# Kernel tuning notes

Measured on AMD Instinct MI355X. Metric: run time of the kernel, lower is better.

The kernel has to match this reference:

```python
import jax, jax.numpy as jnp
import numpy as np

K = 3  # knnLoss default k


def _knn_loss(source_pc, target_pc, k=K):
    """Faithful translation of knnLoss.forward.

    For each batch: drop exact-zero (0,0,0) points from both clouds
    (emulated via masking for static shapes), find the k nearest *target*
    points for every *source* point (query=source, ref=target), take the
    mean Euclidean distance, then average over batch.
    """

    def per_batch(src, tgt):  # src, tgt: [N, 3]
        src_valid = jnp.any(src != 0.0, axis=-1)  # [Ns] move_zero_point mask
        tgt_valid = jnp.any(tgt != 0.0, axis=-1)  # [Nt]
        s2 = jnp.sum(src * src, axis=-1)          # [Ns]
        t2 = jnp.sum(tgt * tgt, axis=-1)          # [Nt]
        # squared pairwise distances, [Ns, Nt]
        d2 = s2[:, None] + t2[None, :] - 2.0 * (src @ tgt.T)
        d2 = jnp.maximum(d2, 0.0)
        # invalid (zero) target points can never be a neighbor
        d2 = jnp.where(tgt_valid[None, :], d2, jnp.inf)
        neg_top, _ = jax.lax.top_k(-d2, k)        # k smallest squared dists
        dist = jnp.sqrt(-neg_top)                 # [Ns, k] euclidean, like KNN_CUDA
        # mean over valid source points x k neighbors
        num = jnp.sum(jnp.where(src_valid[:, None], dist, 0.0))
        den = jnp.sum(src_valid).astype(dist.dtype) * k
        return num / den

    return jnp.mean(jax.vmap(per_batch)(source_pc, target_pc))


def setup_inputs() -> dict:
    key = jax.random.key(0)
    k1, k2 = jax.random.split(key)
    B, N = 4, 8192
    source_pc = jax.random.normal(k1, (B, N, 3), dtype=jnp.float32)
    target_pc = jax.random.normal(k2, (B, N, 3), dtype=jnp.float32)
    return {"source_pc": source_pc, "target_pc": target_pc}


def reference(source_pc, target_pc):
    return _knn_loss(source_pc, target_pc)
```

## Files before the change

### kernel.cpp

```cpp
#include <hip/hip_runtime.h>
#include <math.h>

#define BATCH 4
#define NPTS 8192
#define TILE 512
#define TSPLIT 16
#define SRC_PER_BLOCK 512
#define SRC_CHUNKS 16
#define NSRC_TOT (BATCH * NPTS)

typedef __attribute__((ext_vector_type(2))) float f2;

__device__ __forceinline__ void insert3(float d, float& a0, float& a1, float& a2) {
    float h = fmaxf(a1, d);
    float m = __builtin_amdgcn_fmed3f(a0, a1, d);
    a2 = fminf(a2, h);
    a1 = m;
    a0 = fminf(a0, d);
}

__device__ __forceinline__ void merge33(float a0, float a1, float a2,
                                        float& b0, float& b1, float& b2) {
    float s0 = fminf(a0, b0);
    float h  = fmaxf(a0, b0);
    float m  = fminf(a1, b1);
    float mm = fminf(a2, b2);
    b1 = fminf(h, m);
    b2 = __builtin_amdgcn_fmed3f(h, m, mm);
    b0 = s0;
}

__global__ __launch_bounds__(256) void knn_partial(const float* __restrict__ src,
                                                   const float* __restrict__ tgt,
                                                   float* __restrict__ part,
                                                   float* __restrict__ hdr) {
    __shared__ float4 ts[TILE / 2 * 2];
    const int tid = threadIdx.x;
    const int sc = blockIdx.x, tc = blockIdx.y, b = blockIdx.z;

    if (sc == 0 && tc == 0 && b == 0 && tid < 16) hdr[tid] = 0.0f;

    {
        const float* tb = tgt + ((size_t)b * NPTS + (size_t)tc * TILE + 2 * tid) * 3;
        float x0 = tb[0], y0 = tb[1], z0 = tb[2];
        float x1 = tb[3], y1 = tb[4], z1 = tb[5];
        float w0 = x0 * x0 + y0 * y0 + z0 * z0;
        float w1 = x1 * x1 + y1 * y1 + z1 * z1;
        if (!(x0 != 0.f || y0 != 0.f || z0 != 0.f)) w0 = 3.0e38f;
        if (!(x1 != 0.f || y1 != 0.f || z1 != 0.f)) w1 = 3.0e38f;
        ts[2 * tid + 0] = make_float4(x0, x1, y0, y1);
        ts[2 * tid + 1] = make_float4(z0, z1, w0, w1);
    }
    __syncthreads();

    f2 nx[2], ny[2], nz[2], s2[2];
    #pragma unroll
    for (int s = 0; s < 2; ++s) {
        int i = sc * SRC_PER_BLOCK + tid + 256 * s;
        const float* sp = src + ((size_t)b * NPTS + i) * 3;
        float ax = sp[0], ay = sp[1], az = sp[2];
        float q = ax * ax + ay * ay + az * az;
        nx[s] = (f2){-2.f * ax, -2.f * ax};
        ny[s] = (f2){-2.f * ay, -2.f * ay};
        nz[s] = (f2){-2.f * az, -2.f * az};
        s2[s] = (f2){q, q};
    }

    float c0[2][2], c1[2][2], c2[2][2];
    #pragma unroll
    for (int s = 0; s < 2; ++s)
        for (int h = 0; h < 2; ++h) { c0[s][h] = c1[s][h] = c2[s][h] = 3e38f; }

    #pragma unroll 4
    for (int e = 0; e < TILE / 2; ++e) {
        float4 p = ts[2 * e + 0];
        float4 q = ts[2 * e + 1];
        f2 xs = (f2){p.x, p.y};
        f2 ys = (f2){p.z, p.w};
        f2 zs = (f2){q.x, q.y};
        f2 ws = (f2){q.z, q.w};
        #pragma unroll
        for (int s = 0; s < 2; ++s) {
            f2 acc = ws + s2[s];
            acc = __builtin_elementwise_fma(zs, nz[s], acc);
            acc = __builtin_elementwise_fma(ys, ny[s], acc);
            acc = __builtin_elementwise_fma(xs, nx[s], acc);
            insert3(acc.x, c0[s][0], c1[s][0], c2[s][0]);
            insert3(acc.y, c0[s][1], c1[s][1], c2[s][1]);
        }
    }

    #pragma unroll
    for (int s = 0; s < 2; ++s) {
        merge33(c0[s][1], c1[s][1], c2[s][1], c0[s][0], c1[s][0], c2[s][0]);
        size_t flat = (size_t)b * NPTS + sc * SRC_PER_BLOCK + tid + 256 * s;
        part[((size_t)tc * 3 + 0) * NSRC_TOT + flat] = c0[s][0];
        part[((size_t)tc * 3 + 1) * NSRC_TOT + flat] = c1[s][0];
        part[((size_t)tc * 3 + 2) * NSRC_TOT + flat] = c2[s][0];
    }
}

__global__ __launch_bounds__(256) void knn_merge(const float* __restrict__ src,
                                                 const float* __restrict__ part,
                                                 float* __restrict__ acc,
                                                 float* __restrict__ cnt,
                                                 unsigned* __restrict__ ticket,
                                                 float* __restrict__ out) {
    const int gid = blockIdx.x * 256 + threadIdx.x;
    const int b = gid >> 13;

    float t0[4], t1[4], t2[4];
    #pragma unroll
    for (int c = 0; c < 4; ++c) { t0[c] = t1[c] = t2[c] = 3e38f; }
    #pragma unroll
    for (int q = 0; q < TSPLIT * 3; ++q)
        insert3(part[(size_t)q * NSRC_TOT + gid], t0[q & 3], t1[q & 3], t2[q & 3]);
    merge33(t0[1], t1[1], t2[1], t0[0], t1[0], t2[0]);
    merge33(t0[3], t1[3], t2[3], t0[2], t1[2], t2[2]);
    merge33(t0[2], t1[2], t2[2], t0[0], t1[0], t2[0]);

    float sx = src[(size_t)gid * 3 + 0];
    float sy = src[(size_t)gid * 3 + 1];
    float sz = src[(size_t)gid * 3 + 2];
    bool valid = (sx != 0.f) || (sy != 0.f) || (sz != 0.f);
    float s = valid ? (sqrtf(fmaxf(t0[0], 0.f)) + sqrtf(fmaxf(t1[0], 0.f)) +
                       sqrtf(fmaxf(t2[0], 0.f)))
                    : 0.f;
    float c = valid ? 1.f : 0.f;

    for (int off = 32; off >= 1; off >>= 1) {
        s += __shfl_down(s, off);
        c += __shfl_down(c, off);
    }
    __shared__ float red_s[4], red_c[4];
    int wave = threadIdx.x >> 6, lane = threadIdx.x & 63;
    if (lane == 0) { red_s[wave] = s; red_c[wave] = c; }
    __syncthreads();
    if (threadIdx.x == 0) {
        atomicAdd(&acc[b], red_s[0] + red_s[1] + red_s[2] + red_s[3]);
        atomicAdd(&cnt[b], red_c[0] + red_c[1] + red_c[2] + red_c[3]);
        __threadfence();
        unsigned t = atomicAdd(ticket, 1u);
        if (t == (unsigned)(gridDim.x - 1)) {
            float loss = 0.f;
            #pragma unroll
            for (int bb = 0; bb < BATCH; ++bb) {
                float as = atomicAdd(&acc[bb], 0.f);
                float ac = atomicAdd(&cnt[bb], 0.f);
                loss += as / (ac * 3.0f);
            }
            out[0] = loss * (1.0f / BATCH);
        }
    }
}

extern "C" void kernel_launch(void* const* d_in, const int* in_sizes, int n_in,
                              void* d_out, int out_size, void* d_ws, size_t ws_size,
                              hipStream_t stream) {
    const float* src = (const float*)d_in[0];
    const float* tgt = (const float*)d_in[1];
    float* out = (float*)d_out;

    float* hdr = (float*)d_ws;
    float* acc = hdr;
    float* cnt = hdr + 4;
    unsigned* ticket = (unsigned*)((char*)d_ws + 32);
    float* part = (float*)((char*)d_ws + 256);

    dim3 g1(SRC_CHUNKS, TSPLIT, BATCH);
    knn_partial<<<g1, 256, 0, stream>>>(src, tgt, part, hdr);

    knn_merge<<<dim3(NSRC_TOT / 256), 256, 0, stream>>>(src, part, acc, cnt, ticket, out);
}
```

Baseline: 116.1 us.

## Split merge across four waves per source group and defer source norm

The merge kernel now gives each block 64 source points and splits their 48 partial candidate lists across four waves, which combine through shared memory before the final reduction. This spreads the loads and insertion work over four times as many blocks. The source squared norm is also dropped from the inner distance loop of the partial kernel and added back at merge time, removing one vector add per pair. The cost is extra shared-memory traffic, a barrier, and four times as many atomic operations on the accumulators and ticket.

Result: slower. 126.0 us (+8.5%).

```diff
diff --git a/kernel.cpp b/kernel.cpp
--- a/kernel.cpp
+++ b/kernel.cpp
@@ -8,6 +8,9 @@
 #define SRC_PER_BLOCK 512
 #define SRC_CHUNKS 16
 #define NSRC_TOT (BATCH * NPTS)
+#define QTOT (TSPLIT * 3)
+#define QGROUPS 4
+#define QPG (QTOT / QGROUPS)
 
 typedef __attribute__((ext_vector_type(2))) float f2;
 
@@ -53,17 +56,15 @@
     }
     __syncthreads();
 
-    f2 nx[2], ny[2], nz[2], s2[2];
+    f2 nx[2], ny[2], nz[2];
     #pragma unroll
     for (int s = 0; s < 2; ++s) {
         int i = sc * SRC_PER_BLOCK + tid + 256 * s;
         const float* sp = src + ((size_t)b * NPTS + i) * 3;
         float ax = sp[0], ay = sp[1], az = sp[2];
-        float q = ax * ax + ay * ay + az * az;
         nx[s] = (f2){-2.f * ax, -2.f * ax};
         ny[s] = (f2){-2.f * ay, -2.f * ay};
         nz[s] = (f2){-2.f * az, -2.f * az};
-        s2[s] = (f2){q, q};
     }
 
     float c0[2][2], c1[2][2], c2[2][2];
@@ -81,8 +82,7 @@
         f2 ws = (f2){q.z, q.w};
         #pragma unroll
         for (int s = 0; s < 2; ++s) {
-            f2 acc = ws + s2[s];
-            acc = __builtin_elementwise_fma(zs, nz[s], acc);
+            f2 acc = __builtin_elementwise_fma(zs, nz[s], ws);
             acc = __builtin_elementwise_fma(ys, ny[s], acc);
             acc = __builtin_elementwise_fma(xs, nx[s], acc);
             insert3(acc.x, c0[s][0], c1[s][0], c2[s][0]);
@@ -106,50 +106,69 @@
                                                  float* __restrict__ cnt,
                                                  unsigned* __restrict__ ticket,
                                                  float* __restrict__ out) {
-    const int gid = blockIdx.x * 256 + threadIdx.x;
+    const int lane = threadIdx.x & 63;
+    const int qg = threadIdx.x >> 6;
+    const int gid = blockIdx.x * 64 + lane;
     const int b = gid >> 13;
 
-    float t0[4], t1[4], t2[4];
+    float v[QPG];
     #pragma unroll
-    for (int c = 0; c < 4; ++c) { t0[c] = t1[c] = t2[c] = 3e38f; }
+    for (int j = 0; j < QPG; ++j)
+        v[j] = part[(size_t)(qg * QPG + j) * NSRC_TOT + gid];
+
+    float t0[2], t1[2], t2[2];
     #pragma unroll
-    for (int q = 0; q < TSPLIT * 3; ++q)
-        insert3(part[(size_t)q * NSRC_TOT + gid], t0[q & 3], t1[q & 3], t2[q & 3]);
+    for (int c = 0; c < 2; ++c) { t0[c] = t1[c] = t2[c] = 3e38f; }
+    #pragma unroll
+    for (int j = 0; j < QPG; ++j)
+        insert3(v[j], t0[j & 1], t1[j & 1], t2[j & 1]);
     merge33(t0[1], t1[1], t2[1], t0[0], t1[0], t2[0]);
-    merge33(t0[3], t1[3], t2[3], t0[2], t1[2], t2[2]);
-    merge33(t0[2], t1[2], t2[2], t0[0], t1[0], t2[0]);
 
-    float sx = src[(size_t)gid * 3 + 0];
-    float sy = src[(size_t)gid * 3 + 1];
-    float sz = src[(size_t)gid * 3 + 2];
-    bool valid = (sx != 0.f) || (sy != 0.f) || (sz != 0.f);
-    float s = valid ? (sqrtf(fmaxf(t0[0], 0.f)) + sqrtf(fmaxf(t1[0], 0.f)) +
-                       sqrtf(fmaxf(t2[0], 0.f)))
-                    : 0.f;
-    float c = valid ? 1.f : 0.f;
+    __shared__ float r0[QGROUPS][64], r1[QGROUPS][64], r2[QGROUPS][64];
+    r0[qg][lane] = t0[0];
+    r1[qg][lane] = t1[0];
+    r2[qg][lane] = t2[0];
 
-    for (int off = 32; off >= 1; off >>= 1) {
-        s += __shfl_down(s, off);
-        c += __shfl_down(c, off);
+    float sx = 0.f, sy = 0.f, sz = 0.f;
+    if (threadIdx.x < 64) {
+        sx = src[(size_t)gid * 3 + 0];
+        sy = src[(size_t)gid * 3 + 1];
+        sz = src[(size_t)gid * 3 + 2];
     }
-    __shared__ float red_s[4], red_c[4];
-    int wave = threadIdx.x >> 6, lane = threadIdx.x & 63;
-    if (lane == 0) { red_s[wave] = s; red_c[wave] = c; }
     __syncthreads();
-    if (threadIdx.x == 0) {
-        atomicAdd(&acc[b], red_s[0] + red_s[1] + red_s[2] + red_s[3]);
-        atomicAdd(&cnt[b], red_c[0] + red_c[1] + red_c[2] + red_c[3]);
-        __threadfence();
-        unsigned t = atomicAdd(ticket, 1u);
-        if (t == (unsigned)(gridDim.x - 1)) {
-            float loss = 0.f;
-            #pragma unroll
-            for (int bb = 0; bb < BATCH; ++bb) {
-                float as = atomicAdd(&acc[bb], 0.f);
-                float ac = atomicAdd(&cnt[bb], 0.f);
-                loss += as / (ac * 3.0f);
+
+    if (threadIdx.x < 64) {
+        float a0 = r0[0][lane], a1 = r1[0][lane], a2 = r2[0][lane];
+        #pragma unroll
+        for (int g = 1; g < QGROUPS; ++g)
+            merge33(r0[g][lane], r1[g][lane], r2[g][lane], a0, a1, a2);
+
+        bool valid = (sx != 0.f) || (sy != 0.f) || (sz != 0.f);
+        float q2 = sx * sx + sy * sy + sz * sz;
+        float s = valid ? (sqrtf(fmaxf(a0 + q2, 0.f)) + sqrtf(fmaxf(a1 + q2, 0.f)) +
+                           sqrtf(fmaxf(a2 + q2, 0.f)))
+                        : 0.f;
+        float c = valid ? 1.f : 0.f;
+
+        for (int off = 32; off >= 1; off >>= 1) {
+            s += __shfl_down(s, off);
+            c += __shfl_down(c, off);
+        }
+        if (lane == 0) {
+            atomicAdd(&acc[b], s);
+            atomicAdd(&cnt[b], c);
+            __threadfence();
+            unsigned t = atomicAdd(ticket, 1u);
+            if (t == (unsigned)(gridDim.x - 1)) {
+                float loss = 0.f;
+                #pragma unroll
+                for (int bb = 0; bb < BATCH; ++bb) {
+                    float as = atomicAdd(&acc[bb], 0.f);
+                    float ac = atomicAdd(&cnt[bb], 0.f);
+                    loss += as / (ac * 3.0f);
+                }
+                out[0] = loss * (1.0f / BATCH);
             }
-            out[0] = loss * (1.0f / BATCH);
         }
     }
 }
@@ -170,5 +189,5 @@
     dim3 g1(SRC_CHUNKS, TSPLIT, BATCH);
     knn_partial<<<g1, 256, 0, stream>>>(src, tgt, part, hdr);
 
-    knn_merge<<<dim3(NSRC_TOT / 256), 256, 0, stream>>>(src, part, acc, cnt, ticket, out);
+    knn_merge<<<dim3(NSRC_TOT / 64), 256, 0, stream>>>(src, part, acc, cnt, ticket, out);
 }
```

## Prune KNN scan with per-octet minima and rescan top three octets

Applied to the files above, without the earlier changes.

The inner loop now reduces each group of eight target points to a single minimum with v_min3. The octet index is packed into the low mantissa bits, and only these minima go through the top-3 insertion. A second pass then rescans the three winning octets exactly to get the true top-3 per tile. The source squared norm moves out of the hot loop and is added in the merge kernel, which saves one add per pair. The trade-offs are a new shared-memory layout padded to 36 floats per octet and some extra LDS reads in the rescan, plus a small loss of precision in the octet ranking from masking mantissa bits.

Measured after the change: 98.78 us. 1.18x faster.

```diff
diff --git a/kernel.cpp b/kernel.cpp
--- a/kernel.cpp
+++ b/kernel.cpp
@@ -8,8 +8,16 @@
 #define SRC_PER_BLOCK 512
 #define SRC_CHUNKS 16
 #define NSRC_TOT (BATCH * NPTS)
+#define NOCT (TILE / 8)
+#define OCTF 36
 
 typedef __attribute__((ext_vector_type(2))) float f2;
+
+__device__ __forceinline__ float min3f(float a, float b, float c) {
+    float d;
+    asm("v_min3_f32 %0, %1, %2, %3" : "=v"(d) : "v"(a), "v"(b), "v"(c));
+    return d;
+}
 
 __device__ __forceinline__ void insert3(float d, float& a0, float& a1, float& a2) {
     float h = fmaxf(a1, d);
@@ -30,11 +38,37 @@
     b0 = s0;
 }
 
+__device__ __forceinline__ void octet_insert(const float4* ob, f2 nx, f2 ny, f2 nz,
+                                             float& c0, float& c1, float& c2) {
+    float4 X0 = ob[0], X1 = ob[1], Y0 = ob[2], Y1 = ob[3];
+    float4 Z0 = ob[4], Z1 = ob[5], W0 = ob[6], W1 = ob[7];
+    f2 pa = __builtin_elementwise_fma((f2){Z0.x, Z0.y}, nz, (f2){W0.x, W0.y});
+    pa = __builtin_elementwise_fma((f2){Y0.x, Y0.y}, ny, pa);
+    pa = __builtin_elementwise_fma((f2){X0.x, X0.y}, nx, pa);
+    f2 pb = __builtin_elementwise_fma((f2){Z0.z, Z0.w}, nz, (f2){W0.z, W0.w});
+    pb = __builtin_elementwise_fma((f2){Y0.z, Y0.w}, ny, pb);
+    pb = __builtin_elementwise_fma((f2){X0.z, X0.w}, nx, pb);
+    f2 pc = __builtin_elementwise_fma((f2){Z1.x, Z1.y}, nz, (f2){W1.x, W1.y});
+    pc = __builtin_elementwise_fma((f2){Y1.x, Y1.y}, ny, pc);
+    pc = __builtin_elementwise_fma((f2){X1.x, X1.y}, nx, pc);
+    f2 pd = __builtin_elementwise_fma((f2){Z1.z, Z1.w}, nz, (f2){W1.z, W1.w});
+    pd = __builtin_elementwise_fma((f2){Y1.z, Y1.w}, ny, pd);
+    pd = __builtin_elementwise_fma((f2){X1.z, X1.w}, nx, pd);
+    insert3(pa.x, c0, c1, c2);
+    insert3(pa.y, c0, c1, c2);
+    insert3(pb.x, c0, c1, c2);
+    insert3(pb.y, c0, c1, c2);
+    insert3(pc.x, c0, c1, c2);
+    insert3(pc.y, c0, c1, c2);
+    insert3(pd.x, c0, c1, c2);
+    insert3(pd.y, c0, c1, c2);
+}
+
 __global__ __launch_bounds__(256) void knn_partial(const float* __restrict__ src,
                                                    const float* __restrict__ tgt,
                                                    float* __restrict__ part,
                                                    float* __restrict__ hdr) {
-    __shared__ float4 ts[TILE / 2 * 2];
+    __shared__ float tsf[NOCT * OCTF];
     const int tid = threadIdx.x;
     const int sc = blockIdx.x, tc = blockIdx.y, b = blockIdx.z;
 
@@ -48,55 +82,74 @@
         float w1 = x1 * x1 + y1 * y1 + z1 * z1;
         if (!(x0 != 0.f || y0 != 0.f || z0 != 0.f)) w0 = 3.0e38f;
         if (!(x1 != 0.f || y1 != 0.f || z1 != 0.f)) w1 = 3.0e38f;
-        ts[2 * tid + 0] = make_float4(x0, x1, y0, y1);
-        ts[2 * tid + 1] = make_float4(z0, z1, w0, w1);
+        int o = tid >> 2;
+        int k = (2 * tid) & 7;
+        int base = o * OCTF + ((k >> 2) << 2) + (k & 3);
+        *(float2*)(tsf + base)      = make_float2(x0, x1);
+        *(float2*)(tsf + base + 8)  = make_float2(y0, y1);
+        *(float2*)(tsf + base + 16) = make_float2(z0, z1);
+        *(float2*)(tsf + base + 24) = make_float2(w0, w1);
     }
     __syncthreads();
 
-    f2 nx[2], ny[2], nz[2], s2[2];
+    f2 nx[2], ny[2], nz[2];
     #pragma unroll
     for (int s = 0; s < 2; ++s) {
         int i = sc * SRC_PER_BLOCK + tid + 256 * s;
         const float* sp = src + ((size_t)b * NPTS + i) * 3;
         float ax = sp[0], ay = sp[1], az = sp[2];
-        float q = ax * ax + ay * ay + az * az;
         nx[s] = (f2){-2.f * ax, -2.f * ax};
         ny[s] = (f2){-2.f * ay, -2.f * ay};
         nz[s] = (f2){-2.f * az, -2.f * az};
-        s2[s] = (f2){q, q};
-    }
-
-    float c0[2][2], c1[2][2], c2[2][2];
-    #pragma unroll
-    for (int s = 0; s < 2; ++s)
-        for (int h = 0; h < 2; ++h) { c0[s][h] = c1[s][h] = c2[s][h] = 3e38f; }
-
-    #pragma unroll 4
-    for (int e = 0; e < TILE / 2; ++e) {
-        float4 p = ts[2 * e + 0];
-        float4 q = ts[2 * e + 1];
-        f2 xs = (f2){p.x, p.y};
-        f2 ys = (f2){p.z, p.w};
-        f2 zs = (f2){q.x, q.y};
-        f2 ws = (f2){q.z, q.w};
+    }
+
+    float q0[2], q1[2], q2c[2];
+    #pragma unroll
+    for (int s = 0; s < 2; ++s) { q0[s] = q1[s] = q2c[s] = 3e38f; }
+
+    const float4* tsv = (const float4*)tsf;
+    #pragma unroll 2
+    for (int o = 0; o < NOCT; ++o) {
+        float4 X0 = tsv[9 * o + 0], X1 = tsv[9 * o + 1];
+        float4 Y0 = tsv[9 * o + 2], Y1 = tsv[9 * o + 3];
+        float4 Z0 = tsv[9 * o + 4], Z1 = tsv[9 * o + 5];
+        float4 W0 = tsv[9 * o + 6], W1 = tsv[9 * o + 7];
         #pragma unroll
         for (int s = 0; s < 2; ++s) {
-            f2 acc = ws + s2[s];
-            acc = __builtin_elementwise_fma(zs, nz[s], acc);
-            acc = __builtin_elementwise_fma(ys, ny[s], acc);
-            acc = __builtin_elementwise_fma(xs, nx[s], acc);
-            insert3(acc.x, c0[s][0], c1[s][0], c2[s][0]);
-            insert3(acc.y, c0[s][1], c1[s][1], c2[s][1]);
+            f2 pa = __builtin_elementwise_fma((f2){Z0.x, Z0.y}, nz[s], (f2){W0.x, W0.y});
+            pa = __builtin_elementwise_fma((f2){Y0.x, Y0.y}, ny[s], pa);
+            pa = __builtin_elementwise_fma((f2){X0.x, X0.y}, nx[s], pa);
+            f2 pb = __builtin_elementwise_fma((f2){Z0.z, Z0.w}, nz[s], (f2){W0.z, W0.w});
+            pb = __builtin_elementwise_fma((f2){Y0.z, Y0.w}, ny[s], pb);
+            pb = __builtin_elementwise_fma((f2){X0.z, X0.w}, nx[s], pb);
+            f2 pc = __builtin_elementwise_fma((f2){Z1.x, Z1.y}, nz[s], (f2){W1.x, W1.y});
+            pc = __builtin_elementwise_fma((f2){Y1.x, Y1.y}, ny[s], pc);
+            pc = __builtin_elementwise_fma((f2){X1.x, X1.y}, nx[s], pc);
+            f2 pd = __builtin_elementwise_fma((f2){Z1.z, Z1.w}, nz[s], (f2){W1.z, W1.w});
+            pd = __builtin_elementwise_fma((f2){Y1.z, Y1.w}, ny[s], pd);
+            pd = __builtin_elementwise_fma((f2){X1.z, X1.w}, nx[s], pd);
+            float m1 = min3f(pa.x, pa.y, pb.x);
+            float m2 = min3f(pb.y, pc.x, pc.y);
+            float m3 = min3f(pd.x, pd.y, m1);
+            float m4 = fminf(m2, m3);
+            unsigned u = (__float_as_uint(m4) & 0xFFFFFFC0u) | (unsigned)o;
+            insert3(__uint_as_float(u), q0[s], q1[s], q2c[s]);
         }
     }
 
     #pragma unroll
     for (int s = 0; s < 2; ++s) {
-        merge33(c0[s][1], c1[s][1], c2[s][1], c0[s][0], c1[s][0], c2[s][0]);
+        float c0 = 3e38f, c1 = 3e38f, c2 = 3e38f;
+        int o0 = (int)(__float_as_uint(q0[s]) & 63u);
+        int o1 = (int)(__float_as_uint(q1[s]) & 63u);
+        int o2 = (int)(__float_as_uint(q2c[s]) & 63u);
+        octet_insert(tsv + 9 * o0, nx[s], ny[s], nz[s], c0, c1, c2);
+        octet_insert(tsv + 9 * o1, nx[s], ny[s], nz[s], c0, c1, c2);
+        octet_insert(tsv + 9 * o2, nx[s], ny[s], nz[s], c0, c1, c2);
         size_t flat = (size_t)b * NPTS + sc * SRC_PER_BLOCK + tid + 256 * s;
-        part[((size_t)tc * 3 + 0) * NSRC_TOT + flat] = c0[s][0];
-        part[((size_t)tc * 3 + 1) * NSRC_TOT + flat] = c1[s][0];
-        part[((size_t)tc * 3 + 2) * NSRC_TOT + flat] = c2[s][0];
+        part[((size_t)tc * 3 + 0) * NSRC_TOT + flat] = c0;
+        part[((size_t)tc * 3 + 1) * NSRC_TOT + flat] = c1;
+        part[((size_t)tc * 3 + 2) * NSRC_TOT + flat] = c2;
     }
 }
 
@@ -123,8 +176,9 @@
     float sy = src[(size_t)gid * 3 + 1];
     float sz = src[(size_t)gid * 3 + 2];
     bool valid = (sx != 0.f) || (sy != 0.f) || (sz != 0.f);
-    float s = valid ? (sqrtf(fmaxf(t0[0], 0.f)) + sqrtf(fmaxf(t1[0], 0.f)) +
-                       sqrtf(fmaxf(t2[0], 0.f)))
+    float qq = sx * sx + sy * sy + sz * sz;
+    float s = valid ? (sqrtf(fmaxf(t0[0] + qq, 0.f)) + sqrtf(fmaxf(t1[0] + qq, 0.f)) +
+                       sqrtf(fmaxf(t2[0] + qq, 0.f)))
                     : 0.f;
     float c = valid ? 1.f : 0.f;
 
```
